# Kernel optimization log

Hardware: AMD Instinct MI355X
Metric: run time of the kernel (lower is better)

Reference implementation:

```python
import jax, jax.numpy as jnp
import numpy as np

KW = 3          # kernel_width
PAD = (KW - 1) // 2


def setup_inputs() -> dict:
    key = jax.random.key(0)
    ks = jax.random.split(key, 7)
    B, QL, KL, QS, KS = 16, 1024, 1024, 512, 512
    q = jax.random.normal(ks[0], (B, QL, QS), dtype=jnp.float32)
    k = jax.random.normal(ks[1], (B, KL, KS), dtype=jnp.float32)
    # torch Linear weights: [out_features, in_features]
    Wk = jax.random.normal(ks[2], (KS * KW, QS), dtype=jnp.float32) * (1.0 / np.sqrt(QS))
    bk = jax.random.normal(ks[3], (KS * KW,), dtype=jnp.float32) * 0.02
    Wb = jax.random.normal(ks[4], (1, QS), dtype=jnp.float32) * (1.0 / np.sqrt(QS))
    bb = jax.random.normal(ks[5], (1,), dtype=jnp.float32) * 0.02
    bias_b = jax.random.normal(ks[6], (1,), dtype=jnp.float32)
    return {"q": q, "k": k, "Wk": Wk, "bk": bk, "Wb": Wb, "bb": bb, "bias_b": bias_b}


def reference(q, k, Wk, bk, Wb, bb, bias_b):
    B, QL, QS = q.shape
    _, KL, KS = k.shape
    # per-query dynamic kernels: [B, QL, KS, KW]
    kernel = (jnp.einsum('biq,oq->bio', q, Wk) + bk).reshape(B, QL, KS, KW)
    # per-query scalar bias: [B, QL]
    bias = (jnp.einsum('biq,oq->bio', q, Wb) + bb)[..., 0]
    # banded multiply-accumulate, equivalent to grouped conv1d with groups=B
    k_pad = jnp.pad(k, ((0, 0), (PAD, PAD), (0, 0)))  # [B, KL+KW-1, KS]
    # windows[b, j, t, c] = k_pad[b, j+t, c]  -> [B, KL, KW, KS]
    windows = jnp.stack([k_pad[:, t:t + KL, :] for t in range(KW)], axis=2)
    scores = jnp.einsum('bict,bjtc->bij', kernel, windows)
    return scores + bias[:, :, None] + bias_b[0]
```

## Files before the change

### kernel.cpp

```cpp
#include <hip/hip_runtime.h>

typedef unsigned short ushort_t;
typedef unsigned int uint32;
typedef __bf16 bf16x8 __attribute__((ext_vector_type(8)));
typedef float f32x4 __attribute__((ext_vector_type(4)));
typedef float f4 __attribute__((ext_vector_type(4)));
typedef unsigned short us4 __attribute__((ext_vector_type(4)));


__device__ __forceinline__ ushort_t f2bf(float f) {
    uint32 u = __builtin_bit_cast(uint32, f);
    u = (u + 0x7fffu + ((u >> 16) & 1u)) >> 16;
    return (ushort_t)u;
}

#define SB0() __builtin_amdgcn_sched_barrier(0)
#define SBAR() __builtin_amdgcn_s_barrier()

#define AS1 __attribute__((address_space(1)))
#define AS3 __attribute__((address_space(3)))

__global__ __launch_bounds__(256) void prep_all(const float* __restrict__ q,
                                                const float* __restrict__ Wb,
                                                const float* __restrict__ bb,
                                                const float* __restrict__ k,
                                                const float* __restrict__ Wk,
                                                const float* __restrict__ bk,
                                                ushort_t* __restrict__ qb,
                                                float* __restrict__ biasw,
                                                ushort_t* __restrict__ kbp,
                                                ushort_t* __restrict__ wkb,
                                                float* __restrict__ bkp) {
    const int tid = threadIdx.x;
    if (blockIdx.x < 4096) {
        const int lane = tid & 63, wid = tid >> 6;
        const int m = blockIdx.x * 4 + wid;
        const float* qrow = q + (size_t)m * 512;

        f4 v0 = *(const f4*)(qrow + lane * 4);
        f4 v1 = *(const f4*)(qrow + 256 + lane * 4);
        f4 w0 = *(const f4*)(Wb + lane * 4);
        f4 w1 = *(const f4*)(Wb + 256 + lane * 4);

        float dot = v0[0]*w0[0] + v0[1]*w0[1] + v0[2]*w0[2] + v0[3]*w0[3]
                  + v1[0]*w1[0] + v1[1]*w1[1] + v1[2]*w1[2] + v1[3]*w1[3];

        us4 o0, o1;
        o0[0]=f2bf(v0[0]); o0[1]=f2bf(v0[1]); o0[2]=f2bf(v0[2]); o0[3]=f2bf(v0[3]);
        o1[0]=f2bf(v1[0]); o1[1]=f2bf(v1[1]); o1[2]=f2bf(v1[2]); o1[3]=f2bf(v1[3]);
        *(us4*)(qb + (size_t)m * 512 + lane * 4) = o0;
        *(us4*)(qb + (size_t)m * 512 + 256 + lane * 4) = o1;

        #pragma unroll
        for (int off = 32; off >= 1; off >>= 1) dot += __shfl_xor(dot, off);
        if (lane == 0) biasw[m] = dot + bb[0];
        return;
    }
    const int gid = (blockIdx.x - 4096) * 256 + tid;
    if (gid < 1536) bkp[gid] = bk[(gid & 511) * 3 + (gid >> 9)];

    const int KG = (16 * 1024 * 512) / 4;
    const int PG = (16 * 2 * 512) / 4;

    if (gid < KG) {
        const int e = gid * 4;
        const int b = e >> 19;
        const int rem = e & ((1 << 19) - 1);
        const int row = rem >> 9, c = rem & 511;
        f4 v = *(const f4*)(k + e);
        us4 o; o[0]=f2bf(v[0]); o[1]=f2bf(v[1]); o[2]=f2bf(v[2]); o[3]=f2bf(v[3]);
        *(us4*)(kbp + ((size_t)b * 1026 + row + 1) * 512 + c) = o;
    } else if (gid < KG + PG) {
        const int p = gid - KG;
        const int b = p >> 8, off = p & 255;
        const int row = (off < 128) ? 0 : 1025;
        const int c = (off & 127) * 4;
        us4 z; z[0]=0; z[1]=0; z[2]=0; z[3]=0;
        *(us4*)(kbp + ((size_t)b * 1026 + row) * 512 + c) = z;
    } else {
        const int w = gid - KG - PG;
        const int n = w >> 7;
        const int c = (w & 127) * 4;
        const int o = (n & 511) * 3 + (n >> 9);
        f4 v = *(const f4*)(Wk + (size_t)o * 512 + c);
        us4 ov; ov[0]=f2bf(v[0]); ov[1]=f2bf(v[1]); ov[2]=f2bf(v[2]); ov[3]=f2bf(v[3]);
        *(us4*)(wkb + (size_t)n * 512 + c) = ov;
    }
}

template<int NINST>
__device__ __forceinline__ void stage_half(const char* base, int ld, char* dst, int tid) {
    #pragma unroll
    for (int inst = 0; inst < NINST; ++inst) {
        const int idx = inst * 512 + tid;
        const int row = idx >> 2;
        const int scol = ((idx & 3) ^ ((row >> 1) & 3)) << 4;
        __builtin_amdgcn_global_load_lds(
            (const AS1 void*)(base + (size_t)row * (size_t)ld + scol),
            (AS3 void*)(dst + (size_t)(inst * 512 + (tid & ~63)) * 16),
            16, 0, 0);
    }
}

#define MFMA_BLK(af, bf, r0, NM)                                             \
    SB0();                                                                   \
    __builtin_amdgcn_s_setprio(1);                                           \
    _Pragma("unroll")                                                        \
    for (int i_ = 0; i_ < (NM); ++i_)                                        \
        _Pragma("unroll")                                                    \
        for (int j_ = 0; j_ < 4; ++j_)                                       \
            acc[(r0) + i_][j_] = __builtin_amdgcn_mfma_f32_16x16x32_bf16(    \
                af[i_], bf[j_], acc[(r0) + i_][j_], 0, 0, 0);                \
    __builtin_amdgcn_s_setprio(0);                                           \
    SB0();

#define VMCNT(n) asm volatile("s_waitcnt vmcnt(" #n ")" ::: "memory")

__global__ __launch_bounds__(512, 2) void gemm1(const ushort_t* __restrict__ qb,
                                                const ushort_t* __restrict__ wkb,
                                                const float* __restrict__ bkp,
                                                ushort_t* __restrict__ coef) {
    __shared__ alignas(16) char lds[147456];
    const int tid = threadIdx.x;
    const int l = tid & 63, wid = tid >> 6;
    const int wr = wid >> 2, wc = wid & 3;
    int bid = blockIdx.x;
    bid = (bid & 7) * 96 + (bid >> 3);
    const int mt = bid & 127, nt = bid >> 7;
    const int mbase = mt * 128, nbase = nt * 256;

    const char* Ag = (const char*)(qb + (size_t)mbase * 512);
    const char* Bg = (const char*)(wkb + (size_t)nbase * 512);

    const int r15 = l & 15, q = l >> 4;
    const int swz = ((q ^ (r15 >> 1)) & 3) << 4;
    const int laneA = (wr * 64 + r15) * 64 + swz;
    const int laneB = (wc * 64 + r15) * 64 + swz;

    f32x4 acc[4][4];
    #pragma unroll
    for (int mi = 0; mi < 4; ++mi)
        #pragma unroll
        for (int ni = 0; ni < 4; ++ni)
            #pragma unroll
            for (int r = 0; r < 4; ++r) acc[mi][ni][r] = 0.f;

    stage_half<1>(Ag, 1024, lds, tid);
    stage_half<2>(Bg, 1024, lds + 16384, tid);
    stage_half<1>(Ag + 64, 1024, lds + 8192, tid);
    stage_half<2>(Bg + 64, 1024, lds + 32768, tid);
    stage_half<1>(Ag + 128, 1024, lds + 49152, tid);
    stage_half<2>(Bg + 128, 1024, lds + 49152 + 16384, tid);
    stage_half<1>(Ag + 192, 1024, lds + 49152 + 8192, tid);
    stage_half<2>(Bg + 192, 1024, lds + 49152 + 32768, tid);
    VMCNT(9);
    SBAR();
    bf16x8 Aa[2], Ab[2], Ba[4], Bb[4];
    #pragma unroll
    for (int i = 0; i < 2; ++i) Aa[i] = *(const bf16x8*)(lds + laneA + i * 1024);
    #pragma unroll
    for (int j = 0; j < 4; ++j) Ba[j] = *(const bf16x8*)(lds + 16384 + laneB + j * 1024);

    for (int t = 0; t < 8; ++t) {
        const char* R  = lds + (t % 3) * 49152;
        const char* Nx = lds + ((t + 1) % 3) * 49152;
        char* W        = lds + ((t + 2) % 3) * 49152;
        const int tn2 = (t + 2 < 8) ? t + 2 : 7;
        const size_t off2 = (size_t)tn2 * 128;

        #pragma unroll
        for (int i = 0; i < 2; ++i) Ab[i] = *(const bf16x8*)(R + laneA + (2 + i) * 1024);
        SB0(); SBAR();
        MFMA_BLK(Aa, Ba, 0, 2)

        stage_half<1>(Ag + off2, 1024, W, tid);
        stage_half<2>(Bg + off2, 1024, W + 16384, tid);
        VMCNT(6);
        SBAR(); SB0();
        #pragma unroll
        for (int i = 0; i < 2; ++i) Aa[i] = *(const bf16x8*)(R + 8192 + laneA + i * 1024);
        #pragma unroll
        for (int j = 0; j < 4; ++j) Bb[j] = *(const bf16x8*)(R + 32768 + laneB + j * 1024);
        MFMA_BLK(Ab, Ba, 2, 2)

        stage_half<1>(Ag + off2 + 64, 1024, W + 8192, tid);
        stage_half<2>(Bg + off2 + 64, 1024, W + 32768, tid);
        #pragma unroll
        for (int i = 0; i < 2; ++i) Ab[i] = *(const bf16x8*)(R + 8192 + laneA + (2 + i) * 1024);
        MFMA_BLK(Aa, Bb, 0, 2)

        VMCNT(6);
        SBAR(); SB0();
        #pragma unroll
        for (int i = 0; i < 2; ++i) Aa[i] = *(const bf16x8*)(Nx + laneA + i * 1024);
        #pragma unroll
        for (int j = 0; j < 4; ++j) Ba[j] = *(const bf16x8*)(Nx + 16384 + laneB + j * 1024);
        MFMA_BLK(Ab, Bb, 2, 2)
    }

    #pragma unroll
    for (int ni = 0; ni < 4; ++ni) {
        const int ncol = nbase + wc * 64 + ni * 16 + r15;
        const float bkv = bkp[ncol];
        #pragma unroll
        for (int mi = 0; mi < 4; ++mi) {
            const int mrow0 = mbase + wr * 64 + mi * 16 + q * 4;
            #pragma unroll
            for (int r = 0; r < 4; ++r)
                coef[(size_t)(mrow0 + r) * 1536 + ncol] = f2bf(acc[mi][ni][r] + bkv);
        }
    }
}

__global__ __launch_bounds__(512, 2) void gemm2(const ushort_t* __restrict__ coef,
                                                const ushort_t* __restrict__ kbp,
                                                const float* __restrict__ biasw,
                                                const float* __restrict__ bias_b,
                                                float* __restrict__ out) {
    __shared__ alignas(16) char lds[131072];
    const int tid = threadIdx.x;
    const int l = tid & 63, wid = tid >> 6;
    const int wr = wid >> 2, wc = wid & 3;
    int bid = blockIdx.x;
    bid = (bid & 7) * 32 + (bid >> 3);
    const int jt = bid & 3, it = (bid >> 2) & 3, b = bid >> 4;
    const int ibase = it * 256, jbase = jt * 256;

    const char* Ag = (const char*)(coef + ((size_t)b * 1024 + ibase) * 1536);
    const char* Bg = (const char*)(kbp + ((size_t)b * 1026 + jbase) * 512);

    const int r15 = l & 15, q = l >> 4;
    const int swz = ((q ^ (r15 >> 1)) & 3) << 4;
    const int laneA = (wr * 128 + r15) * 64 + swz;
    const int laneB = (wc * 64 + r15) * 64 + swz;

    f32x4 acc[8][4];
    #pragma unroll
    for (int mi = 0; mi < 8; ++mi)
        #pragma unroll
        for (int ni = 0; ni < 4; ++ni)
            #pragma unroll
            for (int r = 0; r < 4; ++r) acc[mi][ni][r] = 0.f;

    stage_half<2>(Ag, 3072, lds, tid);
    stage_half<2>(Bg, 1024, lds + 32768, tid);
    stage_half<2>(Ag + 64, 3072, lds + 16384, tid);
    stage_half<2>(Bg + 64, 1024, lds + 49152, tid);
    VMCNT(4);
    SBAR();
    bf16x8 Aa[4], Ab[4], Ba[4], Bb[4];
    #pragma unroll
    for (int i = 0; i < 4; ++i) Aa[i] = *(const bf16x8*)(lds + laneA + i * 1024);
    #pragma unroll
    for (int j = 0; j < 4; ++j) Ba[j] = *(const bf16x8*)(lds + 32768 + laneB + j * 1024);

    for (int t = 0; t < 24; ++t) {
        const char* R = lds + ((t & 1) << 16);
        char* W       = lds + (((t + 1) & 1) << 16);
        const int tn = (t < 23) ? t + 1 : t;
        const size_t aoff = (size_t)tn * 128;
        const size_t boff = (size_t)(tn >> 3) * 1024 + (size_t)(tn & 7) * 128;

        #pragma unroll
        for (int i = 0; i < 4; ++i) Ab[i] = *(const bf16x8*)(R + laneA + (4 + i) * 1024);
        SB0(); SBAR();
        MFMA_BLK(Aa, Ba, 0, 4)

        stage_half<2>(Ag + aoff, 3072, W, tid);
        stage_half<2>(Bg + boff, 1024, W + 32768, tid);
        VMCNT(4);
        SBAR(); SB0();
        #pragma unroll
        for (int i = 0; i < 4; ++i) Aa[i] = *(const bf16x8*)(R + 16384 + laneA + i * 1024);
        #pragma unroll
        for (int j = 0; j < 4; ++j) Bb[j] = *(const bf16x8*)(R + 49152 + laneB + j * 1024);
        MFMA_BLK(Ab, Ba, 4, 4)

        stage_half<2>(Ag + aoff + 64, 3072, W + 16384, tid);
        stage_half<2>(Bg + boff + 64, 1024, W + 49152, tid);
        #pragma unroll
        for (int i = 0; i < 4; ++i) Ab[i] = *(const bf16x8*)(R + 16384 + laneA + (4 + i) * 1024);
        MFMA_BLK(Aa, Bb, 0, 4)

        VMCNT(4);
        SBAR(); SB0();
        #pragma unroll
        for (int i = 0; i < 4; ++i) Aa[i] = *(const bf16x8*)(W + laneA + i * 1024);
        #pragma unroll
        for (int j = 0; j < 4; ++j) Ba[j] = *(const bf16x8*)(W + 32768 + laneB + j * 1024);
        MFMA_BLK(Ab, Bb, 4, 4)
    }

    const float bb0v = bias_b[0];
    #pragma unroll
    for (int mi = 0; mi < 8; ++mi) {
        const int irow0 = ibase + wr * 128 + mi * 16 + q * 4;
        #pragma unroll
        for (int r = 0; r < 4; ++r) {
            const float bv = biasw[b * 1024 + irow0 + r] + bb0v;
            #pragma unroll
            for (int ni = 0; ni < 4; ++ni) {
                const int jcol = jbase + wc * 64 + ni * 16 + r15;
                out[((size_t)b << 20) + (size_t)(irow0 + r) * 1024 + jcol] = acc[mi][ni][r] + bv;
            }
        }
    }
}

extern "C" void kernel_launch(void* const* d_in, const int* in_sizes, int n_in,
                              void* d_out, int out_size, void* d_ws, size_t ws_size,
                              hipStream_t stream) {
    const float* q      = (const float*)d_in[0];
    const float* k      = (const float*)d_in[1];
    const float* Wk     = (const float*)d_in[2];
    const float* bk     = (const float*)d_in[3];
    const float* Wb     = (const float*)d_in[4];
    const float* bb     = (const float*)d_in[5];
    const float* bias_b = (const float*)d_in[6];
    float* out = (float*)d_out;

    ushort_t* ws   = (ushort_t*)d_ws;
    ushort_t* qb   = ws;
    ushort_t* kbp  = qb  + (size_t)16384 * 512;
    ushort_t* wkb  = kbp + (size_t)16 * 1026 * 512;
    ushort_t* coef = wkb + (size_t)1536 * 512;
    float*    biasw = (float*)(coef + (size_t)16384 * 1536);
    float*    bkp   = biasw + 16384;

    prep_all<<<13072, 256, 0, stream>>>(q, Wb, bb, k, Wk, bk, qb, biasw, kbp, wkb, bkp);
    gemm1<<<768, 512, 0, stream>>>(qb, wkb, bkp, coef);
    gemm2<<<256, 512, 0, stream>>>(coef, kbp, biasw, bias_b, out);
}
```

Before: 217.4 us.

## Restructure GEMM main loops into barrier-separated load-then-MFMA clusters

Both GEMM kernels drop the software-pipelined register double buffering (Aa/Ab, Ba/Bb prefetched across MFMA blocks). Each K-subtile now loads its fragments from LDS, issues the next global-to-LDS stage, waits on a barrier plus lgkmcnt(0), then runs a 16-MFMA cluster. gemm2 splits the B fragments into two halves so each cluster reuses all 8 A fragments against 2 B fragments. This cuts register pressure and makes the schedule simpler and more explicit, at the cost of exposing LDS read latency before every MFMA cluster and adding more barriers per iteration.

Measured after the change: 211.8 us. 2.6% less time.

```diff
diff --git a/kernel.cpp b/kernel.cpp
--- a/kernel.cpp
+++ b/kernel.cpp
@@ -16,6 +16,8 @@
 
 #define SB0() __builtin_amdgcn_sched_barrier(0)
 #define SBAR() __builtin_amdgcn_s_barrier()
+#define VMCNT(n) asm volatile("s_waitcnt vmcnt(" #n ")" ::: "memory")
+#define LGKM0_SB() do { asm volatile("s_waitcnt lgkmcnt(0)" ::: "memory"); SB0(); } while (0)
 
 #define AS1 __attribute__((address_space(1)))
 #define AS3 __attribute__((address_space(3)))
@@ -102,19 +104,27 @@
     }
 }
 
-#define MFMA_BLK(af, bf, r0, NM)                                             \
-    SB0();                                                                   \
+#define CLUSTER16_G2(AF, BF, njb)                                            \
     __builtin_amdgcn_s_setprio(1);                                           \
     _Pragma("unroll")                                                        \
-    for (int i_ = 0; i_ < (NM); ++i_)                                        \
+    for (int i_ = 0; i_ < 8; ++i_)                                           \
+        _Pragma("unroll")                                                    \
+        for (int j_ = 0; j_ < 2; ++j_)                                       \
+            acc[i_][(njb) + j_] = __builtin_amdgcn_mfma_f32_16x16x32_bf16(   \
+                AF[i_], BF[j_], acc[i_][(njb) + j_], 0, 0, 0);               \
+    __builtin_amdgcn_s_setprio(0);                                           \
+    SB0();
+
+#define CLUSTER16_G1(AF, BF)                                                 \
+    __builtin_amdgcn_s_setprio(1);                                           \
+    _Pragma("unroll")                                                        \
+    for (int i_ = 0; i_ < 4; ++i_)                                           \
         _Pragma("unroll")                                                    \
         for (int j_ = 0; j_ < 4; ++j_)                                       \
-            acc[(r0) + i_][j_] = __builtin_amdgcn_mfma_f32_16x16x32_bf16(    \
-                af[i_], bf[j_], acc[(r0) + i_][j_], 0, 0, 0);                \
+            acc[i_][j_] = __builtin_amdgcn_mfma_f32_16x16x32_bf16(           \
+                AF[i_], BF[j_], acc[i_][j_], 0, 0, 0);                       \
     __builtin_amdgcn_s_setprio(0);                                           \
     SB0();
-
-#define VMCNT(n) asm volatile("s_waitcnt vmcnt(" #n ")" ::: "memory")
 
 __global__ __launch_bounds__(512, 2) void gemm1(const ushort_t* __restrict__ qb,
                                                 const ushort_t* __restrict__ wkb,
@@ -154,48 +164,36 @@
     stage_half<1>(Ag + 192, 1024, lds + 49152 + 8192, tid);
     stage_half<2>(Bg + 192, 1024, lds + 49152 + 32768, tid);
     VMCNT(9);
-    SBAR();
-    bf16x8 Aa[2], Ab[2], Ba[4], Bb[4];
-    #pragma unroll
-    for (int i = 0; i < 2; ++i) Aa[i] = *(const bf16x8*)(lds + laneA + i * 1024);
-    #pragma unroll
-    for (int j = 0; j < 4; ++j) Ba[j] = *(const bf16x8*)(lds + 16384 + laneB + j * 1024);
+    SBAR(); SB0();
 
     for (int t = 0; t < 8; ++t) {
-        const char* R  = lds + (t % 3) * 49152;
-        const char* Nx = lds + ((t + 1) % 3) * 49152;
-        char* W        = lds + ((t + 2) % 3) * 49152;
+        const char* R = lds + (t % 3) * 49152;
+        char* W       = lds + ((t + 2) % 3) * 49152;
         const int tn2 = (t + 2 < 8) ? t + 2 : 7;
         const size_t off2 = (size_t)tn2 * 128;
 
-        #pragma unroll
-        for (int i = 0; i < 2; ++i) Ab[i] = *(const bf16x8*)(R + laneA + (2 + i) * 1024);
-        SB0(); SBAR();
-        MFMA_BLK(Aa, Ba, 0, 2)
-
+        bf16x8 A0[4], B0[4];
+        #pragma unroll
+        for (int i = 0; i < 4; ++i) A0[i] = *(const bf16x8*)(R + laneA + i * 1024);
+        #pragma unroll
+        for (int j = 0; j < 4; ++j) B0[j] = *(const bf16x8*)(R + 16384 + laneB + j * 1024);
         stage_half<1>(Ag + off2, 1024, W, tid);
         stage_half<2>(Bg + off2, 1024, W + 16384, tid);
-        VMCNT(6);
-        SBAR(); SB0();
-        #pragma unroll
-        for (int i = 0; i < 2; ++i) Aa[i] = *(const bf16x8*)(R + 8192 + laneA + i * 1024);
-        #pragma unroll
-        for (int j = 0; j < 4; ++j) Bb[j] = *(const bf16x8*)(R + 32768 + laneB + j * 1024);
-        MFMA_BLK(Ab, Ba, 2, 2)
-
+        VMCNT(9);
+        SBAR();
+        LGKM0_SB();
+        CLUSTER16_G1(A0, B0)
+
+        #pragma unroll
+        for (int i = 0; i < 4; ++i) A0[i] = *(const bf16x8*)(R + 8192 + laneA + i * 1024);
+        #pragma unroll
+        for (int j = 0; j < 4; ++j) B0[j] = *(const bf16x8*)(R + 32768 + laneB + j * 1024);
         stage_half<1>(Ag + off2 + 64, 1024, W + 8192, tid);
         stage_half<2>(Bg + off2 + 64, 1024, W + 32768, tid);
-        #pragma unroll
-        for (int i = 0; i < 2; ++i) Ab[i] = *(const bf16x8*)(R + 8192 + laneA + (2 + i) * 1024);
-        MFMA_BLK(Aa, Bb, 0, 2)
-
-        VMCNT(6);
-        SBAR(); SB0();
-        #pragma unroll
-        for (int i = 0; i < 2; ++i) Aa[i] = *(const bf16x8*)(Nx + laneA + i * 1024);
-        #pragma unroll
-        for (int j = 0; j < 4; ++j) Ba[j] = *(const bf16x8*)(Nx + 16384 + laneB + j * 1024);
-        MFMA_BLK(Ab, Bb, 2, 2)
+        VMCNT(9);
+        SBAR();
+        LGKM0_SB();
+        CLUSTER16_G1(A0, B0)
     }
 
     #pragma unroll
@@ -247,12 +245,7 @@
     stage_half<2>(Ag + 64, 3072, lds + 16384, tid);
     stage_half<2>(Bg + 64, 1024, lds + 49152, tid);
     VMCNT(4);
-    SBAR();
-    bf16x8 Aa[4], Ab[4], Ba[4], Bb[4];
-    #pragma unroll
-    for (int i = 0; i < 4; ++i) Aa[i] = *(const bf16x8*)(lds + laneA + i * 1024);
-    #pragma unroll
-    for (int j = 0; j < 4; ++j) Ba[j] = *(const bf16x8*)(lds + 32768 + laneB + j * 1024);
+    SBAR(); SB0();
 
     for (int t = 0; t < 24; ++t) {
         const char* R = lds + ((t & 1) << 16);
@@ -261,34 +254,40 @@
         const size_t aoff = (size_t)tn * 128;
         const size_t boff = (size_t)(tn >> 3) * 1024 + (size_t)(tn & 7) * 128;
 
-        #pragma unroll
-        for (int i = 0; i < 4; ++i) Ab[i] = *(const bf16x8*)(R + laneA + (4 + i) * 1024);
-        SB0(); SBAR();
-        MFMA_BLK(Aa, Ba, 0, 4)
-
+        bf16x8 A0[8], B0[2], B1[2];
+        #pragma unroll
+        for (int i = 0; i < 8; ++i) A0[i] = *(const bf16x8*)(R + laneA + i * 1024);
+        B0[0] = *(const bf16x8*)(R + 32768 + laneB);
+        B0[1] = *(const bf16x8*)(R + 32768 + laneB + 1024);
         stage_half<2>(Ag + aoff, 3072, W, tid);
+        SBAR();
+        LGKM0_SB();
+        CLUSTER16_G2(A0, B0, 0)
+
+        B1[0] = *(const bf16x8*)(R + 32768 + laneB + 2048);
+        B1[1] = *(const bf16x8*)(R + 32768 + laneB + 3072);
         stage_half<2>(Bg + boff, 1024, W + 32768, tid);
         VMCNT(4);
-        SBAR(); SB0();
-        #pragma unroll
-        for (int i = 0; i < 4; ++i) Aa[i] = *(const bf16x8*)(R + 16384 + laneA + i * 1024);
-        #pragma unroll
-        for (int j = 0; j < 4; ++j) Bb[j] = *(const bf16x8*)(R + 49152 + laneB + j * 1024);
-        MFMA_BLK(Ab, Ba, 4, 4)
-
+        SBAR();
+        LGKM0_SB();
+        CLUSTER16_G2(A0, B1, 2)
+
+        #pragma unroll
+        for (int i = 0; i < 8; ++i) A0[i] = *(const bf16x8*)(R + 16384 + laneA + i * 1024);
+        B0[0] = *(const bf16x8*)(R + 49152 + laneB);
+        B0[1] = *(const bf16x8*)(R + 49152 + laneB + 1024);
         stage_half<2>(Ag + aoff + 64, 3072, W + 16384, tid);
+        SBAR();
+        LGKM0_SB();
+        CLUSTER16_G2(A0, B0, 0)
+
+        B1[0] = *(const bf16x8*)(R + 49152 + laneB + 2048);
+        B1[1] = *(const bf16x8*)(R + 49152 + laneB + 3072);
         stage_half<2>(Bg + boff + 64, 1024, W + 49152, tid);
-        #pragma unroll
-        for (int i = 0; i < 4; ++i) Ab[i] = *(const bf16x8*)(R + 16384 + laneA + (4 + i) * 1024);
-        MFMA_BLK(Aa, Bb, 0, 4)
-
         VMCNT(4);
-        SBAR(); SB0();
-        #pragma unroll
-        for (int i = 0; i < 4; ++i) Aa[i] = *(const bf16x8*)(W + laneA + i * 1024);
-        #pragma unroll
-        for (int j = 0; j < 4; ++j) Ba[j] = *(const bf16x8*)(W + 32768 + laneB + j * 1024);
-        MFMA_BLK(Ab, Bb, 4, 4)
+        SBAR();
+        LGKM0_SB();
+        CLUSTER16_G2(A0, B1, 2)
     }
 
     const float bb0v = bias_b[0];
```
